# Performance work log

Measured on AMD Instinct MI355X. Metric: run time of the kernel, lower is better.

The kernel has to match this reference:

```python
import jax, jax.numpy as jnp
import numpy as np

N = 50000        # num nodes
E = 800000       # num edges (before self-loops)
IN = 256         # in_channels
HID = 32         # hidden_channels per head
HEADS = 8
OUT = 64         # out_channels (layer 2, heads=1)
NEG_SLOPE = 0.2  # PyG GATConv default leaky_relu slope


def setup_inputs() -> dict:
    key = jax.random.key(0)
    ks = jax.random.split(key, 12)
    def rn(k, shape, scale=0.1):
        return jax.random.normal(k, shape, dtype=jnp.float32) * scale
    x = jax.random.normal(ks[0], (N, IN), dtype=jnp.float32)
    edge_index = jax.random.randint(ks[1], (2, E), 0, N, dtype=jnp.int64)
    return {
        "x": x,
        "edge_index": edge_index,
        # GATConv 1: in=256 -> 32 per head, 8 heads, concat
        "W1": rn(ks[2], (IN, HEADS * HID)),
        "att_src1": rn(ks[3], (HEADS, HID)),
        "att_dst1": rn(ks[4], (HEADS, HID)),
        "b1": jnp.zeros((HEADS * HID,), jnp.float32),
        # GATConv 2: in=256 -> 64, 1 head
        "W2": rn(ks[5], (HEADS * HID, OUT)),
        "att_src2": rn(ks[6], (1, OUT)),
        "att_dst2": rn(ks[7], (1, OUT)),
        "b2": jnp.zeros((OUT,), jnp.float32),
    }


def _gat_conv(x, src, dst, W, att_src, att_dst, bias, heads, out_ch):
    """PyG-style GATConv (add_self_loops already applied to src/dst).
    x: [N, F_in]; src/dst: [E']; returns [N, heads*out_ch] (concat)."""
    n = x.shape[0]
    h = (x @ W).reshape(n, heads, out_ch)                     # [N,H,F]
    a_src = jnp.einsum('nhf,hf->nh', h, att_src)              # [N,H]
    a_dst = jnp.einsum('nhf,hf->nh', h, att_dst)
    e = jax.nn.leaky_relu(a_src[src] + a_dst[dst], NEG_SLOPE)  # [E',H]
    # scatter-softmax over incoming edges of each dst node
    m = jax.ops.segment_max(e, dst, num_segments=n)            # [N,H]
    ex = jnp.exp(e - m[dst])
    denom = jax.ops.segment_sum(ex, dst, num_segments=n)       # [N,H]
    alpha = ex / denom[dst]                                    # [E',H]
    msg = alpha[:, :, None] * h[src]                           # [E',H,F]
    out = jax.ops.segment_sum(msg, dst, num_segments=n)        # [N,H,F]
    return out.reshape(n, heads * out_ch) + bias


def reference(x, edge_index, W1, att_src1, att_dst1, b1, W2, att_src2, att_dst2, b2):
    n = x.shape[0]
    loop = jnp.arange(n, dtype=edge_index.dtype)
    src = jnp.concatenate([edge_index[0], loop])  # add self-loops (PyG default)
    dst = jnp.concatenate([edge_index[1], loop])
    h = _gat_conv(x, src, dst, W1, att_src1, att_dst1, b1, HEADS, HID)
    h = jax.nn.relu(h)
    out = _gat_conv(h, src, dst, W2, att_src2, att_dst2, b2, 1, OUT)
    return out
```

## Files before the change

### kernel.cpp

```cpp
#include <hip/hip_runtime.h>
#include <hip/hip_bf16.h>


#define HEADS 8
#define HID 32
#define F1 256
#define F2 64
#define NEG_SLOPE 0.2f
#define SCAN_CHUNK 1024

typedef __attribute__((ext_vector_type(8))) short bf16x8;
typedef __attribute__((ext_vector_type(4))) float f32x4;
typedef __attribute__((ext_vector_type(8))) unsigned short u16x8;

__device__ __forceinline__ unsigned short f2b(float f) {
    union { float f; unsigned int i; } x; x.f = f;
    unsigned int r = x.i + 0x7fffu + ((x.i >> 16) & 1u);
    return (unsigned short)(r >> 16);
}
__device__ __forceinline__ float b2f(unsigned short u) {
    union { unsigned int i; float f; } x; x.i = ((unsigned int)u) << 16;
    return x.f;
}
__device__ __forceinline__ float leaky(float v) {
    return v > 0.f ? v : NEG_SLOPE * v;
}

__global__ void setup_kernel(const float* __restrict__ W1,
                             const float* __restrict__ W2,
                             unsigned short* __restrict__ W1T,
                             unsigned short* __restrict__ W2T,
                             int* __restrict__ deg, int Nn) {
    const int i = blockIdx.x * 256 + threadIdx.x;
    if (i < F1 * F1) {
        const int k = i >> 8, n = i & (F1 - 1);
        W1T[(size_t)n * F1 + k] = f2b(W1[i]);
    } else if (i < F1 * F1 + F1 * F2) {
        const int j = i - F1 * F1;
        const int k = j >> 6, n = j & (F2 - 1);
        W2T[(size_t)n * F1 + k] = f2b(W2[j]);
    } else if (i < F1 * F1 + F1 * F2 + Nn) {
        deg[i - F1 * F1 - F1 * F2] = 0;
    }
}

template<int BN, bool A_FP32, int OUT_MODE>
__global__ __launch_bounds__(256) void mfma_gemm(
        const void* __restrict__ A,
        const unsigned short* __restrict__ BT,
        void* __restrict__ C, int M, int N, int K) {
    constexpr int BM = 128, BK = 32;
    __shared__ unsigned short As[BM * BK];
    __shared__ unsigned short Bs[BN * BK];
    const int tid = threadIdx.x;
    const int wave = tid >> 6, lane = tid & 63;
    const int quad = lane >> 4, l16 = lane & 15;
    const int brow = blockIdx.x * BM;
    const int bcol = blockIdx.y * BN;

    constexpr int MI = (BN == 128) ? 4 : 2;
    constexpr int NJ = 4;
    const int wm = (BN == 128) ? (wave & 1) * 64 : wave * 32;
    const int wn = (BN == 128) ? (wave >> 1) * 64 : 0;

    f32x4 acc[MI][NJ] = {};

    for (int k0 = 0; k0 < K; k0 += BK) {
#pragma unroll
        for (int it = 0; it < (BM * BK) / (256 * 8); ++it) {
            const int idx = it * 256 + tid;
            const int r = idx >> 2;
            const int kk = (idx & 3) * 8;
            const int gr = brow + r;
            if (A_FP32) {
                const float* Af = (const float*)A;
                float4 a0 = make_float4(0.f, 0.f, 0.f, 0.f);
                float4 a1 = make_float4(0.f, 0.f, 0.f, 0.f);
                if (gr < M) {
                    a0 = *(const float4*)&Af[(size_t)gr * K + k0 + kk];
                    a1 = *(const float4*)&Af[(size_t)gr * K + k0 + kk + 4];
                }
                ushort4 lo, hi;
                lo.x = f2b(a0.x); lo.y = f2b(a0.y); lo.z = f2b(a0.z); lo.w = f2b(a0.w);
                hi.x = f2b(a1.x); hi.y = f2b(a1.y); hi.z = f2b(a1.z); hi.w = f2b(a1.w);
                *(ushort4*)&As[r * BK + kk] = lo;
                *(ushort4*)&As[r * BK + kk + 4] = hi;
            } else {
                const unsigned short* Ab = (const unsigned short*)A;
                uint4 v = make_uint4(0u, 0u, 0u, 0u);
                if (gr < M) v = *(const uint4*)&Ab[(size_t)gr * K + k0 + kk];
                *(uint4*)&As[r * BK + kk] = v;
            }
        }
#pragma unroll
        for (int it = 0; it < (BN * BK) / (256 * 8); ++it) {
            const int idx = it * 256 + tid;
            const int r = idx >> 2;
            const int kk = (idx & 3) * 8;
            const uint4 v = *(const uint4*)&BT[(size_t)(bcol + r) * K + k0 + kk];
            *(uint4*)&Bs[r * BK + kk] = v;
        }
        __syncthreads();
        bf16x8 af[MI], bfr[NJ];
#pragma unroll
        for (int i = 0; i < MI; ++i)
            af[i] = *(const bf16x8*)&As[(wm + i * 16 + l16) * BK + quad * 8];
#pragma unroll
        for (int j = 0; j < NJ; ++j)
            bfr[j] = *(const bf16x8*)&Bs[(wn + j * 16 + l16) * BK + quad * 8];
#pragma unroll
        for (int i = 0; i < MI; ++i)
#pragma unroll
            for (int j = 0; j < NJ; ++j)
                acc[i][j] = __builtin_amdgcn_mfma_f32_16x16x32_bf16(
                    af[i], bfr[j], acc[i][j], 0, 0, 0);
        __syncthreads();
    }
#pragma unroll
    for (int i = 0; i < MI; ++i) {
#pragma unroll
        for (int r = 0; r < 4; ++r) {
            const int row = brow + wm + i * 16 + quad * 4 + r;
            if (row >= M) continue;
#pragma unroll
            for (int j = 0; j < NJ; ++j) {
                const int col = bcol + wn + j * 16 + l16;
                const float v = acc[i][j][r];
                if (OUT_MODE == 0) {
                    ((float*)C)[(size_t)row * N + col] = v;
                } else if (OUT_MODE == 1) {
                    ((unsigned short*)C)[(size_t)row * N + col] = f2b(v);
                } else {
                    ((unsigned short*)C)[((size_t)(col >> 5) * M + row) * HID
                                         + (col & 31)] = f2b(v);
                }
            }
        }
    }
}

__global__ void att1_kernel(const unsigned short* __restrict__ h1hm,
                            const float* __restrict__ att_src,
                            const float* __restrict__ att_dst,
                            float* __restrict__ a_src,
                            float* __restrict__ a_dst, int Nn) {
    const int n = blockIdx.x * blockDim.x + threadIdx.x;
    const int h = blockIdx.y;
    if (n >= Nn) return;
    const unsigned short* hp = h1hm + ((size_t)h * Nn + n) * HID;
    const float* as = att_src + h * HID;
    const float* ad = att_dst + h * HID;
    float s = 0.f, d = 0.f;
#pragma unroll
    for (int f = 0; f < HID; ++f) {
        const float v = b2f(hp[f]);
        s += v * as[f];
        d += v * ad[f];
    }
    a_src[(size_t)h * Nn + n] = s;
    a_dst[(size_t)h * Nn + n] = d;
}

__global__ void att2_kernel(const unsigned short* __restrict__ h2b,
                            const float* __restrict__ att_src,
                            const float* __restrict__ att_dst,
                            float* __restrict__ a_src,
                            float* __restrict__ a_dst, int Nn) {
    const int n = blockIdx.x * blockDim.x + threadIdx.x;
    if (n >= Nn) return;
    const unsigned short* hp = h2b + (size_t)n * F2;
    float s = 0.f, d = 0.f;
#pragma unroll
    for (int f = 0; f < F2; ++f) {
        const float v = b2f(hp[f]);
        s += v * att_src[f];
        d += v * att_dst[f];
    }
    a_src[n] = s;
    a_dst[n] = d;
}

__global__ void hist_kernel(const int* __restrict__ ei, int E,
                            int* __restrict__ deg) {
    const int e = blockIdx.x * blockDim.x + threadIdx.x;
    if (e < E) atomicAdd(&deg[ei[E + e]], 1);
}

__global__ __launch_bounds__(256) void scan_bsum(const int* __restrict__ deg,
                                                 int* __restrict__ bsum, int Nn) {
    const int base = blockIdx.x * SCAN_CHUNK + threadIdx.x * 4;
    int s = 0;
#pragma unroll
    for (int j = 0; j < 4; ++j) {
        const int i = base + j;
        if (i < Nn) s += deg[i];
    }
#pragma unroll
    for (int off = 32; off > 0; off >>= 1) s += __shfl_down(s, off, 64);
    __shared__ int ws[4];
    if ((threadIdx.x & 63) == 0) ws[threadIdx.x >> 6] = s;
    __syncthreads();
    if (threadIdx.x == 0) bsum[blockIdx.x] = ws[0] + ws[1] + ws[2] + ws[3];
}

__global__ __launch_bounds__(256) void scan_boff(const int* __restrict__ bsum,
                                                 int* __restrict__ boff,
                                                 int* __restrict__ rowptr,
                                                 int B, int Nn) {
    __shared__ int sums[256];
    const int tid = threadIdx.x;
    const int v = (tid < B) ? bsum[tid] : 0;
    sums[tid] = v;
    __syncthreads();
    for (int off = 1; off < 256; off <<= 1) {
        const int cur = sums[tid];
        const int add = (tid >= off) ? sums[tid - off] : 0;
        __syncthreads();
        sums[tid] = cur + add;
        __syncthreads();
    }
    if (tid < B) boff[tid] = sums[tid] - v;
    if (tid == 255) rowptr[Nn] = sums[255];
}

__global__ __launch_bounds__(256) void scan_write(const int* __restrict__ deg,
                                                  const int* __restrict__ boff,
                                                  int* __restrict__ rowptr,
                                                  int* __restrict__ cursor, int Nn) {
    const int tid = threadIdx.x;
    const int base = blockIdx.x * SCAN_CHUNK + tid * 4;
    int v[4];
    int s = 0;
#pragma unroll
    for (int j = 0; j < 4; ++j) {
        const int i = base + j;
        v[j] = (i < Nn) ? deg[i] : 0;
        s += v[j];
    }
    __shared__ int sums[256];
    sums[tid] = s;
    __syncthreads();
    for (int off = 1; off < 256; off <<= 1) {
        const int cur = sums[tid];
        const int add = (tid >= off) ? sums[tid - off] : 0;
        __syncthreads();
        sums[tid] = cur + add;
        __syncthreads();
    }
    int off = boff[blockIdx.x] + sums[tid] - s;
#pragma unroll
    for (int j = 0; j < 4; ++j) {
        const int i = base + j;
        if (i < Nn) {
            rowptr[i] = off;
            cursor[i] = off;
            off += v[j];
        }
    }
}

__global__ void scatter_kernel(const int* __restrict__ ei, int E,
                               int* __restrict__ cursor,
                               int* __restrict__ csr_src) {
    const int e = blockIdx.x * blockDim.x + threadIdx.x;
    if (e >= E) return;
    const int d = ei[E + e];
    const int pos = atomicAdd(&cursor[d], 1);
    csr_src[pos] = ei[e];
}

__global__ __launch_bounds__(256) void gather1_kernel(
        const int* __restrict__ rowptr, const int* __restrict__ csr_src,
        const float* __restrict__ a_src, const float* __restrict__ a_dst,
        const unsigned short* __restrict__ h1hm, const float* __restrict__ b1,
        unsigned short* __restrict__ out1b, int Nn) {
    const int h = blockIdx.x & 7;
    const int lane = threadIdx.x & 63;
    const int wave = threadIdx.x >> 6;
    const int sub = lane >> 3;
    const int cl  = lane & 7;
    const int d = (blockIdx.x >> 3) * 32 + wave * 8 + sub;
    if (d >= Nn) return;

    const unsigned short* hh = h1hm + (size_t)h * Nn * HID;
    const float* asrc = a_src + (size_t)h * Nn;
    const float adst = a_dst[(size_t)h * Nn + d];

    float denom, a0, a1, a2, a3;
    {
        const float w = __expf(leaky(asrc[d] + adst));
        const ushort4 v = *(const ushort4*)&hh[(size_t)d * HID + cl * 4];
        denom = w;
        a0 = w * b2f(v.x); a1 = w * b2f(v.y);
        a2 = w * b2f(v.z); a3 = w * b2f(v.w);
    }
    const int beg = rowptr[d], end = rowptr[d + 1];
    for (int i = beg; i < end; i += 4) {
        int s[4];
        float e[4];
        ushort4 vv[4];
        bool ok[4];
#pragma unroll
        for (int j = 0; j < 4; ++j) {
            ok[j] = (i + j) < end;
            s[j] = ok[j] ? csr_src[i + j] : d;
        }
#pragma unroll
        for (int j = 0; j < 4; ++j) e[j] = asrc[s[j]];
#pragma unroll
        for (int j = 0; j < 4; ++j)
            vv[j] = *(const ushort4*)&hh[(size_t)s[j] * HID + cl * 4];
#pragma unroll
        for (int j = 0; j < 4; ++j) {
            float w = __expf(leaky(e[j] + adst));
            w = ok[j] ? w : 0.f;
            denom += w;
            a0 += w * b2f(vv[j].x); a1 += w * b2f(vv[j].y);
            a2 += w * b2f(vv[j].z); a3 += w * b2f(vv[j].w);
        }
    }
    const float inv = 1.f / denom;
    const int c = h * HID + cl * 4;
    ushort4 o;
    o.x = f2b(fmaxf(a0 * inv + b1[c + 0], 0.f));
    o.y = f2b(fmaxf(a1 * inv + b1[c + 1], 0.f));
    o.z = f2b(fmaxf(a2 * inv + b1[c + 2], 0.f));
    o.w = f2b(fmaxf(a3 * inv + b1[c + 3], 0.f));
    *(ushort4*)&out1b[(size_t)d * F1 + c] = o;
}

__global__ __launch_bounds__(256) void gather2_kernel(
        const int* __restrict__ rowptr, const int* __restrict__ csr_src,
        const float* __restrict__ a_src, const float* __restrict__ a_dst,
        const unsigned short* __restrict__ h2b, const float* __restrict__ b2,
        float* __restrict__ out, int Nn) {
    const int lane = threadIdx.x & 63;
    const int sub  = lane >> 4;
    const int l    = lane & 15;
    int d = blockIdx.x * 16 + (threadIdx.x >> 6) * 4 + sub;
    const bool valid = d < Nn;
    if (!valid) d = Nn - 1;
    const int c = l * 4;

    const float adst = a_dst[d];
    float a0, a1, a2, a3, denom;
    {
        const float w = __expf(leaky(a_src[d] + adst));
        const ushort4 v = *(const ushort4*)&h2b[(size_t)d * F2 + c];
        denom = w;
        a0 = w * b2f(v.x); a1 = w * b2f(v.y);
        a2 = w * b2f(v.z); a3 = w * b2f(v.w);
    }
    const int beg = rowptr[d], end = rowptr[d + 1];
    int i = beg;
    for (; i + 4 <= end; i += 4) {
        int s[4];
        float e[4];
        ushort4 vv[4];
#pragma unroll
        for (int jj = 0; jj < 4; ++jj) s[jj] = csr_src[i + jj];
#pragma unroll
        for (int jj = 0; jj < 4; ++jj) e[jj] = a_src[s[jj]];
#pragma unroll
        for (int jj = 0; jj < 4; ++jj)
            vv[jj] = *(const ushort4*)&h2b[(size_t)s[jj] * F2 + c];
#pragma unroll
        for (int jj = 0; jj < 4; ++jj) {
            const float w = __expf(leaky(e[jj] + adst));
            denom += w;
            a0 += w * b2f(vv[jj].x); a1 += w * b2f(vv[jj].y);
            a2 += w * b2f(vv[jj].z); a3 += w * b2f(vv[jj].w);
        }
    }
    for (; i < end; ++i) {
        const int s = csr_src[i];
        const float w = __expf(leaky(a_src[s] + adst));
        const ushort4 v = *(const ushort4*)&h2b[(size_t)s * F2 + c];
        denom += w;
        a0 += w * b2f(v.x); a1 += w * b2f(v.y);
        a2 += w * b2f(v.z); a3 += w * b2f(v.w);
    }
    if (valid) {
        const float inv = 1.f / denom;
        float4 o;
        o.x = a0 * inv + b2[c + 0];
        o.y = a1 * inv + b2[c + 1];
        o.z = a2 * inv + b2[c + 2];
        o.w = a3 * inv + b2[c + 3];
        *(float4*)&out[(size_t)d * F2 + c] = o;
    }
}

extern "C" void kernel_launch(void* const* d_in, const int* in_sizes, int n_in,
                              void* d_out, int out_size, void* d_ws, size_t ws_size,
                              hipStream_t stream) {
    const float* x        = (const float*)d_in[0];
    const int*   ei       = (const int*)d_in[1];
    const float* W1       = (const float*)d_in[2];
    const float* att_src1 = (const float*)d_in[3];
    const float* att_dst1 = (const float*)d_in[4];
    const float* b1       = (const float*)d_in[5];
    const float* W2       = (const float*)d_in[6];
    const float* att_src2 = (const float*)d_in[7];
    const float* att_dst2 = (const float*)d_in[8];
    const float* b2       = (const float*)d_in[9];
    float* out = (float*)d_out;

    const int Nn = in_sizes[0] / F1;
    const int E  = in_sizes[1] / 2;
    const int NB = (Nn + SCAN_CHUNK - 1) / SCAN_CHUNK;

    char* p = (char*)d_ws;
    unsigned short* h1hm  = (unsigned short*)p; p += (size_t)Nn * F1 * 2;
    unsigned short* out1b = (unsigned short*)p; p += (size_t)Nn * F1 * 2;
    unsigned short* W1T   = (unsigned short*)p; p += (size_t)F1 * F1 * 2;
    unsigned short* W2T   = (unsigned short*)p; p += (size_t)F2 * F1 * 2;
    unsigned short* h2b   = (unsigned short*)p; p += (size_t)Nn * F2 * 2;
    float* a_src1 = (float*)p; p += (size_t)Nn * HEADS * 4;
    float* a_dst1 = (float*)p; p += (size_t)Nn * HEADS * 4;
    float* a_src2 = (float*)p; p += (size_t)Nn * 4;
    float* a_dst2 = (float*)p; p += (size_t)Nn * 4;
    int* deg     = (int*)p; p += (size_t)Nn * 4;
    int* rowptr  = (int*)p; p += (size_t)(Nn + 1) * 4;
    int* cursor  = (int*)p; p += (size_t)Nn * 4;
    int* bsum    = (int*)p; p += 256 * 4;
    int* boff    = (int*)p; p += 256 * 4;
    int* csr_src = (int*)p; p += (size_t)E * 4;

    {
        const int total = F1 * F1 + F1 * F2 + Nn;
        setup_kernel<<<(total + 255) / 256, 256, 0, stream>>>(
            W1, W2, W1T, W2T, deg, Nn);
    }

    hist_kernel<<<(E + 255) / 256, 256, 0, stream>>>(ei, E, deg);
    scan_bsum<<<NB, 256, 0, stream>>>(deg, bsum, Nn);
    scan_boff<<<1, 256, 0, stream>>>(bsum, boff, rowptr, NB, Nn);
    scan_write<<<NB, 256, 0, stream>>>(deg, boff, rowptr, cursor, Nn);
    scatter_kernel<<<(E + 255) / 256, 256, 0, stream>>>(ei, E, cursor, csr_src);

    {
        dim3 grid((Nn + 127) / 128, F1 / 128);
        mfma_gemm<128, true, 2><<<grid, 256, 0, stream>>>(
            x, W1T, h1hm, Nn, F1, F1);
    }
    {
        dim3 grid((Nn + 255) / 256, HEADS);
        att1_kernel<<<grid, 256, 0, stream>>>(
            h1hm, att_src1, att_dst1, a_src1, a_dst1, Nn);
    }
    gather1_kernel<<<((Nn + 31) / 32) * 8, 256, 0, stream>>>(
        rowptr, csr_src, a_src1, a_dst1, h1hm, b1, out1b, Nn);

    {
        dim3 grid((Nn + 127) / 128, F2 / 64);
        mfma_gemm<64, false, 1><<<grid, 256, 0, stream>>>(
            out1b, W2T, h2b, Nn, F2, F1);
    }
    att2_kernel<<<(Nn + 255) / 256, 256, 0, stream>>>(
        h2b, att_src2, att_dst2, a_src2, a_dst2, Nn);
    gather2_kernel<<<(Nn + 15) / 16, 256, 0, stream>>>(
        rowptr, csr_src, a_src2, a_dst2, h2b, b2, out, Nn);
}
```

Baseline: 339.9 us.

## Pad CSR rows to multiples of four and precompute layer-1 edge weights

```diff
diff --git a/kernel.cpp b/kernel.cpp
--- a/kernel.cpp
+++ b/kernel.cpp
@@ -11,7 +11,6 @@
 
 typedef __attribute__((ext_vector_type(8))) short bf16x8;
 typedef __attribute__((ext_vector_type(4))) float f32x4;
-typedef __attribute__((ext_vector_type(8))) unsigned short u16x8;
 
 __device__ __forceinline__ unsigned short f2b(float f) {
     union { float f; unsigned int i; } x; x.f = f;
@@ -30,7 +29,9 @@
                              const float* __restrict__ W2,
                              unsigned short* __restrict__ W1T,
                              unsigned short* __restrict__ W2T,
-                             int* __restrict__ deg, int Nn) {
+                             int* __restrict__ deg,
+                             int* __restrict__ csr_src,
+                             int Nn, int Epad) {
     const int i = blockIdx.x * 256 + threadIdx.x;
     if (i < F1 * F1) {
         const int k = i >> 8, n = i & (F1 - 1);
@@ -41,6 +42,8 @@
         W2T[(size_t)n * F1 + k] = f2b(W2[j]);
     } else if (i < F1 * F1 + F1 * F2 + Nn) {
         deg[i - F1 * F1 - F1 * F2] = 0;
+    } else if (i < F1 * F1 + F1 * F2 + Nn + Epad) {
+        csr_src[i - F1 * F1 - F1 * F2 - Nn] = -1;
     }
 }
 
@@ -193,7 +196,7 @@
 #pragma unroll
     for (int j = 0; j < 4; ++j) {
         const int i = base + j;
-        if (i < Nn) s += deg[i];
+        if (i < Nn) s += (deg[i] + 3) & ~3;
     }
 #pragma unroll
     for (int off = 32; off > 0; off >>= 1) s += __shfl_down(s, off, 64);
@@ -234,7 +237,7 @@
 #pragma unroll
     for (int j = 0; j < 4; ++j) {
         const int i = base + j;
-        v[j] = (i < Nn) ? deg[i] : 0;
+        v[j] = (i < Nn) ? ((deg[i] + 3) & ~3) : 0;
         s += v[j];
     }
     __shared__ int sums[256];
@@ -261,34 +264,55 @@
 
 __global__ void scatter_kernel(const int* __restrict__ ei, int E,
                                int* __restrict__ cursor,
-                               int* __restrict__ csr_src) {
+                               int* __restrict__ csr_src,
+                               int* __restrict__ csr_dst) {
     const int e = blockIdx.x * blockDim.x + threadIdx.x;
     if (e >= E) return;
     const int d = ei[E + e];
     const int pos = atomicAdd(&cursor[d], 1);
     csr_src[pos] = ei[e];
+    csr_dst[pos] = d;
+}
+
+__global__ void wt1_kernel(const int* __restrict__ csr_src,
+                           const int* __restrict__ csr_dst,
+                           const float* __restrict__ a_src,
+                           const float* __restrict__ a_dst,
+                           float* __restrict__ wt, int Epad, int Nn) {
+    const int i = blockIdx.x * 256 + threadIdx.x;
+    if (i >= Epad) return;
+    const int h = blockIdx.y;
+    const int s = csr_src[i];
+    const int dd = csr_dst[i];
+    const bool ok = s >= 0;
+    const int ss = ok ? s : 0;
+    const int ds = ok ? dd : 0;
+    const float e = a_src[(size_t)h * Nn + ss] + a_dst[(size_t)h * Nn + ds];
+    const float w = __expf(leaky(e));
+    wt[(size_t)h * Epad + i] = ok ? w : 0.f;
 }
 
 __global__ __launch_bounds__(256) void gather1_kernel(
         const int* __restrict__ rowptr, const int* __restrict__ csr_src,
+        const float* __restrict__ wt,
         const float* __restrict__ a_src, const float* __restrict__ a_dst,
         const unsigned short* __restrict__ h1hm, const float* __restrict__ b1,
-        unsigned short* __restrict__ out1b, int Nn) {
+        unsigned short* __restrict__ out1b, int Nn, int Epad) {
     const int h = blockIdx.x & 7;
     const int lane = threadIdx.x & 63;
-    const int wave = threadIdx.x >> 6;
+    const int wv = threadIdx.x >> 6;
     const int sub = lane >> 3;
     const int cl  = lane & 7;
-    const int d = (blockIdx.x >> 3) * 32 + wave * 8 + sub;
+    const int d = (blockIdx.x >> 3) * 32 + wv * 8 + sub;
     if (d >= Nn) return;
 
     const unsigned short* hh = h1hm + (size_t)h * Nn * HID;
-    const float* asrc = a_src + (size_t)h * Nn;
-    const float adst = a_dst[(size_t)h * Nn + d];
+    const float* wth = wt + (size_t)h * Epad;
 
     float denom, a0, a1, a2, a3;
     {
-        const float w = __expf(leaky(asrc[d] + adst));
+        const float adst = a_dst[(size_t)h * Nn + d];
+        const float w = __expf(leaky(a_src[(size_t)h * Nn + d] + adst));
         const ushort4 v = *(const ushort4*)&hh[(size_t)d * HID + cl * 4];
         denom = w;
         a0 = w * b2f(v.x); a1 = w * b2f(v.y);
@@ -296,28 +320,28 @@
     }
     const int beg = rowptr[d], end = rowptr[d + 1];
     for (int i = beg; i < end; i += 4) {
-        int s[4];
-        float e[4];
-        ushort4 vv[4];
-        bool ok[4];
-#pragma unroll
-        for (int j = 0; j < 4; ++j) {
-            ok[j] = (i + j) < end;
-            s[j] = ok[j] ? csr_src[i + j] : d;
-        }
-#pragma unroll
-        for (int j = 0; j < 4; ++j) e[j] = asrc[s[j]];
-#pragma unroll
-        for (int j = 0; j < 4; ++j)
-            vv[j] = *(const ushort4*)&hh[(size_t)s[j] * HID + cl * 4];
-#pragma unroll
-        for (int j = 0; j < 4; ++j) {
-            float w = __expf(leaky(e[j] + adst));
-            w = ok[j] ? w : 0.f;
-            denom += w;
-            a0 += w * b2f(vv[j].x); a1 += w * b2f(vv[j].y);
-            a2 += w * b2f(vv[j].z); a3 += w * b2f(vv[j].w);
-        }
+        const int4 s4 = *(const int4*)&csr_src[i];
+        const float4 w4 = *(const float4*)&wth[i];
+        const int s0 = s4.x < 0 ? 0 : s4.x;
+        const int s1 = s4.y < 0 ? 0 : s4.y;
+        const int s2 = s4.z < 0 ? 0 : s4.z;
+        const int s3 = s4.w < 0 ? 0 : s4.w;
+        const ushort4 v0 = *(const ushort4*)&hh[(size_t)s0 * HID + cl * 4];
+        const ushort4 v1 = *(const ushort4*)&hh[(size_t)s1 * HID + cl * 4];
+        const ushort4 v2 = *(const ushort4*)&hh[(size_t)s2 * HID + cl * 4];
+        const ushort4 v3 = *(const ushort4*)&hh[(size_t)s3 * HID + cl * 4];
+        denom += w4.x;
+        a0 += w4.x * b2f(v0.x); a1 += w4.x * b2f(v0.y);
+        a2 += w4.x * b2f(v0.z); a3 += w4.x * b2f(v0.w);
+        denom += w4.y;
+        a0 += w4.y * b2f(v1.x); a1 += w4.y * b2f(v1.y);
+        a2 += w4.y * b2f(v1.z); a3 += w4.y * b2f(v1.w);
+        denom += w4.z;
+        a0 += w4.z * b2f(v2.x); a1 += w4.z * b2f(v2.y);
+        a2 += w4.z * b2f(v2.z); a3 += w4.z * b2f(v2.w);
+        denom += w4.w;
+        a0 += w4.w * b2f(v3.x); a1 += w4.w * b2f(v3.y);
+        a2 += w4.w * b2f(v3.z); a3 += w4.w * b2f(v3.w);
     }
     const float inv = 1.f / denom;
     const int c = h * HID + cl * 4;
@@ -352,33 +376,25 @@
         a2 = w * b2f(v.z); a3 = w * b2f(v.w);
     }
     const int beg = rowptr[d], end = rowptr[d + 1];
-    int i = beg;
-    for (; i + 4 <= end; i += 4) {
-        int s[4];
+    for (int i = beg; i < end; i += 4) {
+        const int4 s4 = *(const int4*)&csr_src[i];
+        int s[4] = { s4.x, s4.y, s4.z, s4.w };
         float e[4];
         ushort4 vv[4];
 #pragma unroll
-        for (int jj = 0; jj < 4; ++jj) s[jj] = csr_src[i + jj];
-#pragma unroll
-        for (int jj = 0; jj < 4; ++jj) e[jj] = a_src[s[jj]];
-#pragma unroll
-        for (int jj = 0; jj < 4; ++jj)
-            vv[jj] = *(const ushort4*)&h2b[(size_t)s[jj] * F2 + c];
-#pragma unroll
         for (int jj = 0; jj < 4; ++jj) {
-            const float w = __expf(leaky(e[jj] + adst));
+            const int ss = s[jj] < 0 ? 0 : s[jj];
+            e[jj] = a_src[ss];
+            vv[jj] = *(const ushort4*)&h2b[(size_t)ss * F2 + c];
+        }
+#pragma unroll
+        for (int jj = 0; jj < 4; ++jj) {
+            float w = __expf(leaky(e[jj] + adst));
+            w = s[jj] < 0 ? 0.f : w;
             denom += w;
             a0 += w * b2f(vv[jj].x); a1 += w * b2f(vv[jj].y);
             a2 += w * b2f(vv[jj].z); a3 += w * b2f(vv[jj].w);
         }
-    }
-    for (; i < end; ++i) {
-        const int s = csr_src[i];
-        const float w = __expf(leaky(a_src[s] + adst));
-        const ushort4 v = *(const ushort4*)&h2b[(size_t)s * F2 + c];
-        denom += w;
-        a0 += w * b2f(v.x); a1 += w * b2f(v.y);
-        a2 += w * b2f(v.z); a3 += w * b2f(v.w);
     }
     if (valid) {
         const float inv = 1.f / denom;
@@ -408,6 +424,7 @@
 
     const int Nn = in_sizes[0] / F1;
     const int E  = in_sizes[1] / 2;
+    const int Epad = E + 4 * Nn;
     const int NB = (Nn + SCAN_CHUNK - 1) / SCAN_CHUNK;
 
     char* p = (char*)d_ws;
@@ -416,6 +433,7 @@
     unsigned short* W1T   = (unsigned short*)p; p += (size_t)F1 * F1 * 2;
     unsigned short* W2T   = (unsigned short*)p; p += (size_t)F2 * F1 * 2;
     unsigned short* h2b   = (unsigned short*)p; p += (size_t)Nn * F2 * 2;
+    float* wt     = (float*)p; p += (size_t)HEADS * Epad * 4;
     float* a_src1 = (float*)p; p += (size_t)Nn * HEADS * 4;
     float* a_dst1 = (float*)p; p += (size_t)Nn * HEADS * 4;
     float* a_src2 = (float*)p; p += (size_t)Nn * 4;
@@ -425,19 +443,21 @@
     int* cursor  = (int*)p; p += (size_t)Nn * 4;
     int* bsum    = (int*)p; p += 256 * 4;
     int* boff    = (int*)p; p += 256 * 4;
-    int* csr_src = (int*)p; p += (size_t)E * 4;
-
-    {
-        const int total = F1 * F1 + F1 * F2 + Nn;
+    int* csr_src = (int*)p; p += (size_t)Epad * 4;
+    int* csr_dst = (int*)p; p += (size_t)Epad * 4;
+
+    {
+        const int total = F1 * F1 + F1 * F2 + Nn + Epad;
         setup_kernel<<<(total + 255) / 256, 256, 0, stream>>>(
-            W1, W2, W1T, W2T, deg, Nn);
+            W1, W2, W1T, W2T, deg, csr_src, Nn, Epad);
     }
 
     hist_kernel<<<(E + 255) / 256, 256, 0, stream>>>(ei, E, deg);
     scan_bsum<<<NB, 256, 0, stream>>>(deg, bsum, Nn);
     scan_boff<<<1, 256, 0, stream>>>(bsum, boff, rowptr, NB, Nn);
     scan_write<<<NB, 256, 0, stream>>>(deg, boff, rowptr, cursor, Nn);
-    scatter_kernel<<<(E + 255) / 256, 256, 0, stream>>>(ei, E, cursor, csr_src);
+    scatter_kernel<<<(E + 255) / 256, 256, 0, stream>>>(
+        ei, E, cursor, csr_src, csr_dst);
 
     {
         dim3 grid((Nn + 127) / 128, F1 / 128);
@@ -449,8 +469,13 @@
         att1_kernel<<<grid, 256, 0, stream>>>(
             h1hm, att_src1, att_dst1, a_src1, a_dst1, Nn);
     }
+    {
+        dim3 grid((Epad + 255) / 256, HEADS);
+        wt1_kernel<<<grid, 256, 0, stream>>>(
+            csr_src, csr_dst, a_src1, a_dst1, wt, Epad, Nn);
+    }
     gather1_kernel<<<((Nn + 31) / 32) * 8, 256, 0, stream>>>(
-        rowptr, csr_src, a_src1, a_dst1, h1hm, b1, out1b, Nn);
+        rowptr, csr_src, wt, a_src1, a_dst1, h1hm, b1, out1b, Nn, Epad);
 
     {
         dim3 grid((Nn + 127) / 128, F2 / 64);
```

After: 369.1 us. +8.6%, slower.
